# Kernel optimization log

Measured on AMD Instinct MI355X. Metric: run time of the kernel, lower is better.

## Reference

```python
import jax, jax.numpy as jnp
import numpy as np

D = 256
N = 131072


def setup_inputs() -> dict:
    key = jax.random.key(0)
    kx, ku = jax.random.split(key)
    X = jax.random.normal(kx, (N, D), dtype=jnp.float32)
    U = jax.random.normal(ku, (D, D), dtype=jnp.float32) * 0.5
    # reset_parameters: normalize each row of U
    U = U / jnp.linalg.norm(U, axis=1, keepdims=True)
    return {"X": X, "U": U}


def reference(X, U):
    # sequential_mult iterates rows from d-1 down to 0, so scan over flipped U.
    def step(Xc, v):
        # v: [d];  X <- X - 2 * (X v) v^T / (v.v)
        coef = (Xc @ v) * (2.0 / jnp.dot(v, v))  # [N]
        Xc = Xc - coef[:, None] * v[None, :]
        return Xc, None

    Xout, _ = jax.lax.scan(step, X, U[::-1])
    return Xout
```

## Files before the change

### kernel.cpp

```cpp
#include <hip/hip_runtime.h>
#include <hip/hip_bf16.h>

typedef __attribute__((ext_vector_type(8))) short short8;
typedef __attribute__((ext_vector_type(4))) float f32x4;

#define DDIM 256
#define NROWS 131072
#define GBLK 512
#define RPB (NROWS / GBLK)

static __device__ __forceinline__ unsigned short f2bf(float f){
  unsigned b = __builtin_bit_cast(unsigned, f);
  b += 0x7FFFu + ((b >> 16) & 1u);
  return (unsigned short)(b >> 16);
}

static __device__ __forceinline__ float wave_sum_bcast(float x){
  int v = __builtin_bit_cast(int, x);
#define DPP_ADD(ctrl)                                                          \
  v = __builtin_bit_cast(int,                                                  \
        __builtin_bit_cast(float, v) +                                         \
        __builtin_bit_cast(float,                                              \
          __builtin_amdgcn_update_dpp(0, v, (ctrl), 0xF, 0xF, true)))
  DPP_ADD(0x111);
  DPP_ADD(0x112);
  DPP_ADD(0x114);
  DPP_ADD(0x118);
  DPP_ADD(0x142);
  DPP_ADD(0x143);
#undef DPP_ADD
  return __builtin_bit_cast(float, __builtin_amdgcn_readlane(v, 63));
}

__global__ __launch_bounds__(256) void compute_beta(const float* __restrict__ U,
                                                    float* __restrict__ beta){
  const int k = threadIdx.x;
  const f32x4* r = reinterpret_cast<const f32x4*>(U + (size_t)k * 256);
  float s0 = 0.f, s1 = 0.f, s2 = 0.f, s3 = 0.f;
#pragma unroll
  for (int i = 0; i < 64; i += 4){
    f32x4 a = r[i], b = r[i + 1], c = r[i + 2], d = r[i + 3];
    s0 += a[0]*a[0] + a[1]*a[1] + a[2]*a[2] + a[3]*a[3];
    s1 += b[0]*b[0] + b[1]*b[1] + b[2]*b[2] + b[3]*b[3];
    s2 += c[0]*c[0] + c[1]*c[1] + c[2]*c[2] + c[3]*c[3];
    s3 += d[0]*d[0] + d[1]*d[1] + d[2]*d[2] + d[3]*d[3];
  }
  beta[k] = 2.0f / ((s0 + s1) + (s2 + s3));
}

__global__ __launch_bounds__(256) void compute_q(const float* __restrict__ U,
                                                 const float* __restrict__ beta,
                                                 unsigned short* __restrict__ Qt){
  const int lane = threadIdx.x & 63;
  const int wv   = threadIdx.x >> 6;
  const int pair = blockIdx.x * 4 + wv;
  const int j0 = pair * 2, j1 = j0 + 1;

  float u0[4], u1[4], r0[4], r1[4], r2[4], r3[4];
#pragma unroll
  for (int e = 0; e < 4; ++e){
    const int i = e * 64 + lane;
    u0[e] = (i == j0) ? 1.f : 0.f;
    u1[e] = (i == j1) ? 1.f : 0.f;
    r0[e] = U[0 * 256 + i];
    r1[e] = U[1 * 256 + i];
    r2[e] = U[2 * 256 + i];
    r3[e] = U[3 * 256 + i];
  }
  float b0 = beta[0], b1 = beta[1], b2 = beta[2], b3 = beta[3];

#define QSTEP(R, B, KN)                                                        \
  do {                                                                         \
    const float p0_ = (u0[0]*R[0] + u0[1]*R[1]) + (u0[2]*R[2] + u0[3]*R[3]);   \
    const float p1_ = (u1[0]*R[0] + u1[1]*R[1]) + (u1[2]*R[2] + u1[3]*R[3]);   \
    const float d0_ = wave_sum_bcast(p0_);                                     \
    const float d1_ = wave_sum_bcast(p1_);                                     \
    const float c0_ = d0_ * B, c1_ = d1_ * B;                                  \
    _Pragma("unroll")                                                          \
    for (int e = 0; e < 4; ++e){                                               \
      u0[e] = fmaf(-c0_, R[e], u0[e]);                                         \
      u1[e] = fmaf(-c1_, R[e], u1[e]);                                         \
      R[e] = U[(size_t)(KN) * 256 + e * 64 + lane];                            \
    }                                                                          \
    B = beta[(KN)];                                                            \
  } while (0)

  for (int k = 0; k < 256; k += 4){
    const int k4 = (k+4) & 255, k5 = (k+5) & 255, k6 = (k+6) & 255, k7 = (k+7) & 255;
    QSTEP(r0, b0, k4);
    QSTEP(r1, b1, k5);
    QSTEP(r2, b2, k6);
    QSTEP(r3, b3, k7);
  }
#undef QSTEP

#pragma unroll
  for (int e = 0; e < 4; ++e){
    const int i = e * 64 + lane;
    Qt[(size_t)j0 * 256 + i] = f2bf(u0[e]);
    Qt[(size_t)j1 * 256 + i] = f2bf(u1[e]);
  }
}

__global__ __launch_bounds__(1024, 4) void gemm_xq(const float* __restrict__ X,
                                                   const unsigned short* __restrict__ Qt,
                                                   float* __restrict__ Y){
  __shared__ char qb[131072];

  const int tid  = threadIdx.x;
  const int lane = tid & 63;
  const int wv   = tid >> 6;
  const int lg   = lane >> 4;
  const int lm   = lane & 15;
  const size_t row0 = (size_t)blockIdx.x * RPB + wv * 16;

  const float* xp = X + (row0 + lm) * DDIM + lg * 8;
  f32x4 xv[16];
#pragma unroll
  for (int kk = 0; kk < 8; ++kk){
    xv[2*kk]   = *reinterpret_cast<const f32x4*>(xp + kk * 32);
    xv[2*kk+1] = *reinterpret_cast<const f32x4*>(xp + kk * 32 + 4);
  }

#pragma unroll
  for (int it = 0; it < 8; ++it){
    const int c   = tid + it * 1024;
    const int n   = c >> 5;
    const int off = (c & 31) << 4;
    const f32x4 d = *reinterpret_cast<const f32x4*>(
        reinterpret_cast<const char*>(Qt) + (n << 9) + off);
    *reinterpret_cast<f32x4*>(qb + (n << 9) + (off ^ ((n & 15) << 5))) = d;
  }
  __syncthreads();

#pragma unroll
  for (int h = 0; h < 2; ++h){
    f32x4 acc[8];
#pragma unroll
    for (int nt = 0; nt < 8; ++nt) acc[nt] = (f32x4){0.f, 0.f, 0.f, 0.f};

#pragma unroll
    for (int kk = 0; kk < 8; ++kk){
      const f32x4 lo = xv[2*kk], hi = xv[2*kk+1];
      short8 a;
      a[0] = (short)f2bf(lo[0]); a[1] = (short)f2bf(lo[1]);
      a[2] = (short)f2bf(lo[2]); a[3] = (short)f2bf(lo[3]);
      a[4] = (short)f2bf(hi[0]); a[5] = (short)f2bf(hi[1]);
      a[6] = (short)f2bf(hi[2]); a[7] = (short)f2bf(hi[3]);

      const int kb = kk * 64 + (lg << 4);
#pragma unroll
      for (int nt = 0; nt < 8; ++nt){
        const int n = h * 128 + nt * 16 + lm;
        const short8 b = *reinterpret_cast<const short8*>(
            qb + (n << 9) + (kb ^ ((n & 15) << 5)));
        acc[nt] = __builtin_amdgcn_mfma_f32_16x16x32_bf16(a, b, acc[nt], 0, 0, 0);
      }
    }

    const size_t orow = row0 + lg * 4;
#pragma unroll
    for (int nt = 0; nt < 8; ++nt){
#pragma unroll
      for (int r = 0; r < 4; ++r){
        Y[(orow + r) * DDIM + h * 128 + nt * 16 + lm] = acc[nt][r];
      }
    }
  }
}

extern "C" void kernel_launch(void* const* d_in, const int* in_sizes, int n_in,
                              void* d_out, int out_size, void* d_ws, size_t ws_size,
                              hipStream_t stream) {
  const float* X = (const float*)d_in[0];
  const float* U = (const float*)d_in[1];
  float* Y = (float*)d_out;
  unsigned short* Qt = (unsigned short*)d_ws;

  float* beta = (float*)d_out + ((size_t)out_size - 256);

  compute_beta<<<1, 256, 0, stream>>>(U, beta);
  compute_q<<<32, 256, 0, stream>>>(U, beta, Qt);
  gemm_xq<<<GBLK, 1024, 0, stream>>>(X, Qt, Y);
}
```

Baseline: 105.0 us.

## Split GEMM output columns across block pairs and parallelize beta norms

Each GEMM block now covers 128 rows and only half of the 256 output columns, with 512 threads and 64KB of LDS holding half of Qt instead of all of it. The Qt global load is issued into registers before the X load so the two can overlap. compute_beta now uses one wave per row with a DPP reduction across 64 blocks rather than a single serial block. This lowers LDS per block so more blocks can be resident, but each X row is now read and converted to bf16 twice.

```diff
diff --git a/kernel.cpp b/kernel.cpp
--- a/kernel.cpp
+++ b/kernel.cpp
@@ -6,8 +6,8 @@
 
 #define DDIM 256
 #define NROWS 131072
-#define GBLK 512
-#define RPB (NROWS / GBLK)
+#define ROWS_PER_BLK 128
+#define GBLK ((NROWS / ROWS_PER_BLK) * 2)
 
 static __device__ __forceinline__ unsigned short f2bf(float f){
   unsigned b = __builtin_bit_cast(unsigned, f);
@@ -34,18 +34,11 @@
 
 __global__ __launch_bounds__(256) void compute_beta(const float* __restrict__ U,
                                                     float* __restrict__ beta){
-  const int k = threadIdx.x;
-  const f32x4* r = reinterpret_cast<const f32x4*>(U + (size_t)k * 256);
-  float s0 = 0.f, s1 = 0.f, s2 = 0.f, s3 = 0.f;
-#pragma unroll
-  for (int i = 0; i < 64; i += 4){
-    f32x4 a = r[i], b = r[i + 1], c = r[i + 2], d = r[i + 3];
-    s0 += a[0]*a[0] + a[1]*a[1] + a[2]*a[2] + a[3]*a[3];
-    s1 += b[0]*b[0] + b[1]*b[1] + b[2]*b[2] + b[3]*b[3];
-    s2 += c[0]*c[0] + c[1]*c[1] + c[2]*c[2] + c[3]*c[3];
-    s3 += d[0]*d[0] + d[1]*d[1] + d[2]*d[2] + d[3]*d[3];
-  }
-  beta[k] = 2.0f / ((s0 + s1) + (s2 + s3));
+  const int lane = threadIdx.x & 63;
+  const int k = blockIdx.x * 4 + (threadIdx.x >> 6);
+  const f32x4 a = *reinterpret_cast<const f32x4*>(U + (size_t)k * 256 + lane * 4);
+  const float s = wave_sum_bcast(a[0]*a[0] + a[1]*a[1] + a[2]*a[2] + a[3]*a[3]);
+  if (lane == 0) beta[k] = 2.0f / s;
 }
 
 __global__ __launch_bounds__(256) void compute_q(const float* __restrict__ U,
@@ -102,17 +95,28 @@
   }
 }
 
-__global__ __launch_bounds__(1024, 4) void gemm_xq(const float* __restrict__ X,
-                                                   const unsigned short* __restrict__ Qt,
-                                                   float* __restrict__ Y){
-  __shared__ char qb[131072];
+__global__ __launch_bounds__(512, 4) void gemm_xq(const float* __restrict__ X,
+                                                  const unsigned short* __restrict__ Qt,
+                                                  float* __restrict__ Y){
+  __shared__ char qb[65536];
 
   const int tid  = threadIdx.x;
   const int lane = tid & 63;
   const int wv   = tid >> 6;
   const int lg   = lane >> 4;
   const int lm   = lane & 15;
-  const size_t row0 = (size_t)blockIdx.x * RPB + wv * 16;
+  const int half = blockIdx.x & 1;
+  const size_t rg = blockIdx.x >> 1;
+  const size_t row0 = rg * ROWS_PER_BLK + wv * 16;
+
+  f32x4 sv[8];
+#pragma unroll
+  for (int it = 0; it < 8; ++it){
+    const int c = tid + it * 512;
+    sv[it] = *reinterpret_cast<const f32x4*>(
+        reinterpret_cast<const char*>(Qt) +
+        ((size_t)(half * 128) << 9) + ((size_t)c << 4));
+  }
 
   const float* xp = X + (row0 + lm) * DDIM + lg * 8;
   f32x4 xv[16];
@@ -124,47 +128,43 @@
 
 #pragma unroll
   for (int it = 0; it < 8; ++it){
-    const int c   = tid + it * 1024;
+    const int c   = tid + it * 512;
     const int n   = c >> 5;
     const int off = (c & 31) << 4;
-    const f32x4 d = *reinterpret_cast<const f32x4*>(
-        reinterpret_cast<const char*>(Qt) + (n << 9) + off);
-    *reinterpret_cast<f32x4*>(qb + (n << 9) + (off ^ ((n & 15) << 5))) = d;
+    *reinterpret_cast<f32x4*>(qb + (n << 9) + (off ^ ((n & 15) << 5))) = sv[it];
   }
   __syncthreads();
 
+  f32x4 acc[8];
 #pragma unroll
-  for (int h = 0; h < 2; ++h){
-    f32x4 acc[8];
-#pragma unroll
-    for (int nt = 0; nt < 8; ++nt) acc[nt] = (f32x4){0.f, 0.f, 0.f, 0.f};
+  for (int nt = 0; nt < 8; ++nt) acc[nt] = (f32x4){0.f, 0.f, 0.f, 0.f};
 
 #pragma unroll
-    for (int kk = 0; kk < 8; ++kk){
-      const f32x4 lo = xv[2*kk], hi = xv[2*kk+1];
-      short8 a;
-      a[0] = (short)f2bf(lo[0]); a[1] = (short)f2bf(lo[1]);
-      a[2] = (short)f2bf(lo[2]); a[3] = (short)f2bf(lo[3]);
-      a[4] = (short)f2bf(hi[0]); a[5] = (short)f2bf(hi[1]);
-      a[6] = (short)f2bf(hi[2]); a[7] = (short)f2bf(hi[3]);
+  for (int kk = 0; kk < 8; ++kk){
+    const f32x4 lo = xv[2*kk], hi = xv[2*kk+1];
+    short8 a;
+    a[0] = (short)f2bf(lo[0]); a[1] = (short)f2bf(lo[1]);
+    a[2] = (short)f2bf(lo[2]); a[3] = (short)f2bf(lo[3]);
+    a[4] = (short)f2bf(hi[0]); a[5] = (short)f2bf(hi[1]);
+    a[6] = (short)f2bf(hi[2]); a[7] = (short)f2bf(hi[3]);
 
-      const int kb = kk * 64 + (lg << 4);
-#pragma unroll
-      for (int nt = 0; nt < 8; ++nt){
-        const int n = h * 128 + nt * 16 + lm;
-        const short8 b = *reinterpret_cast<const short8*>(
-            qb + (n << 9) + (kb ^ ((n & 15) << 5)));
-        acc[nt] = __builtin_amdgcn_mfma_f32_16x16x32_bf16(a, b, acc[nt], 0, 0, 0);
-      }
-    }
-
-    const size_t orow = row0 + lg * 4;
+    const int kb = kk * 64 + (lg << 4);
 #pragma unroll
     for (int nt = 0; nt < 8; ++nt){
+      const int nl = nt * 16 + lm;
+      const short8 b = *reinterpret_cast<const short8*>(
+          qb + (nl << 9) + (kb ^ ((nl & 15) << 5)));
+      acc[nt] = __builtin_amdgcn_mfma_f32_16x16x32_bf16(a, b, acc[nt], 0, 0, 0);
+    }
+  }
+
+  const size_t orow = row0 + lg * 4;
+  const int col0 = half * 128;
 #pragma unroll
-      for (int r = 0; r < 4; ++r){
-        Y[(orow + r) * DDIM + h * 128 + nt * 16 + lm] = acc[nt][r];
-      }
+  for (int nt = 0; nt < 8; ++nt){
+#pragma unroll
+    for (int r = 0; r < 4; ++r){
+      Y[(orow + r) * DDIM + col0 + nt * 16 + lm] = acc[nt][r];
     }
   }
 }
@@ -179,7 +179,7 @@
 
   float* beta = (float*)d_out + ((size_t)out_size - 256);
 
-  compute_beta<<<1, 256, 0, stream>>>(U, beta);
+  compute_beta<<<64, 256, 0, stream>>>(U, beta);
   compute_q<<<32, 256, 0, stream>>>(U, beta, Qt);
-  gemm_xq<<<GBLK, 1024, 0, stream>>>(X, Qt, Y);
+  gemm_xq<<<GBLK, 512, 0, stream>>>(X, Qt, Y);
 }
```

Result: slower. 110.9 us (+5.7%).
